# Kernel tuning notes

Hardware: AMD Instinct MI355X
Metric: run time of the kernel (lower is better)

The kernel has to match this reference:

```python
import jax, jax.numpy as jnp
import numpy as np

N, E, F, H, C, L = 50000, 800000, 32, 4, 32, 3
HC = H * C
NEG = 0.2  # leaky_relu negative slope (GATv2Conv default and explicit LeakyReLU(0.2))


def _gat_layer(x, src, dst, ea, Wl, bl, Wr, br, att, We, cb, lW, lb, bsc, bsh):
    # GATv2 linear transforms: [N, F] -> [N, H, C]
    xl = (x @ Wl + bl).reshape(N, H, C)
    xr = (x @ Wr + br).reshape(N, H, C)
    xj = xl[src]            # [E, H, C] messages from source nodes
    xi = xr[dst]            # [E, H, C] target-side features
    ep = (ea[:, None] @ We).reshape(E, H, C)  # edge-linear, edge_dim=1
    e = jax.nn.leaky_relu(xi + xj + ep, NEG)
    logits = jnp.einsum('ehc,hc->eh', e, att)            # [E, H]
    # segment softmax over destination node neighborhoods
    m = jax.ops.segment_max(logits, dst, num_segments=N)
    a = jnp.exp(logits - m[dst])
    denom = jax.ops.segment_sum(a, dst, num_segments=N)
    alpha = a / denom[dst]                               # [E, H]
    msg = xj * alpha[..., None]                          # [E, H, C]
    out = jax.ops.segment_sum(msg, dst, num_segments=N).reshape(N, HC) + cb
    # trailing per-layer MLP: Linear -> LeakyReLU(0.2) -> BatchNorm1d (eval, affine)
    h = jax.nn.leaky_relu(out @ lW + lb, NEG)
    return h * bsc + bsh


def setup_inputs() -> dict:
    key = jax.random.key(0)
    ks = jax.random.split(key, 24)
    s = 0.1
    inp = {
        'x': jax.random.normal(ks[0], (N, F), jnp.float32),
        'edge_index': jax.random.randint(ks[1], (2, E), 0, N, jnp.int32),
        'edge_attr': jax.random.normal(ks[2], (E,), jnp.float32),
        'batch': jnp.zeros((N,), jnp.int32),
        # stacked per-layer conv params (all 3 layers share shapes: F==hidden)
        'Wl': jax.random.normal(ks[3], (L, F, HC), jnp.float32) * s,
        'bl': jnp.zeros((L, HC), jnp.float32),
        'Wr': jax.random.normal(ks[4], (L, F, HC), jnp.float32) * s,
        'br': jnp.zeros((L, HC), jnp.float32),
        'att': jax.random.normal(ks[5], (L, H, C), jnp.float32) * s,
        'We': jax.random.normal(ks[6], (L, 1, HC), jnp.float32) * s,
        'conv_b': jnp.zeros((L, HC), jnp.float32),
        'lin_W': jax.random.normal(ks[7], (L, HC, F), jnp.float32) * s,
        'lin_b': jnp.zeros((L, F), jnp.float32),
        'bn_scale': jnp.ones((L, F), jnp.float32),
        'bn_shift': jnp.zeros((L, F), jnp.float32),
        # fcn head: hidden -> 256 -> 32 -> num_classes
        'W1': jax.random.normal(ks[8], (F, 256), jnp.float32) * s,
        'b1': jnp.zeros((256,), jnp.float32),
        'W2': jax.random.normal(ks[9], (256, 32), jnp.float32) * s,
        'b2': jnp.zeros((32,), jnp.float32),
        'W3': jax.random.normal(ks[10], (32, 2), jnp.float32) * s,
        'b3': jnp.zeros((2,), jnp.float32),
    }
    return inp


def reference(x, edge_index, edge_attr, batch, Wl, bl, Wr, br, att, We, conv_b,
              lin_W, lin_b, bn_scale, bn_shift, W1, b1, W2, b2, W3, b3):
    src, dst = edge_index[0], edge_index[1]
    ea = jnp.abs(edge_attr)
    h = x
    for i in range(L):
        h = _gat_layer(h, src, dst, ea, Wl[i], bl[i], Wr[i], br[i], att[i],
                       We[i], conv_b[i], lin_W[i], lin_b[i], bn_scale[i], bn_shift[i])
    # global mean pool over graphs in batch (single graph here, B=1)
    B = 1
    sums = jax.ops.segment_sum(h, batch, num_segments=B)
    cnts = jax.ops.segment_sum(jnp.ones((N, 1), h.dtype), batch, num_segments=B)
    g = sums / cnts
    g = jax.nn.leaky_relu(g @ W1 + b1, NEG)
    g = jax.nn.leaky_relu(g @ W2 + b2, NEG)
    return g @ W3 + b3
```

## Files before the change

kernel.cpp:

```cpp
#include <hip/hip_runtime.h>
#include <hip/hip_bf16.h>
#include <math.h>

#define NN 50000
#define EE 800000
#define HC 128
#define FF 32
#define NEG 0.2f
#define CAP 64
#define LOG2E 1.4426950408889634f


__global__ void k_bucket(const int* __restrict__ src, const int* __restrict__ dst,
                         const float* __restrict__ ea, int* __restrict__ cnt,
                         int2* __restrict__ pairs) {
    int e = blockIdx.x * 256 + threadIdx.x;
    if (e >= EE) return;
    int d = dst[e];
    int pos = atomicAdd(&cnt[d], 1);
    pairs[d * CAP + pos] = make_int2(src[e], __float_as_int(fabsf(ea[e])));
}


__global__ void k_hist(const int* __restrict__ dst, int* __restrict__ deg) {
    int e = blockIdx.x * 256 + threadIdx.x;
    if (e < EE) atomicAdd(&deg[dst[e]], 1);
}

__global__ void k_scan1(const int* __restrict__ deg, int* __restrict__ part) {
    __shared__ int sd[256];
    int b = blockIdx.x, t = threadIdx.x;
    int base = b * 1024 + t * 4;
    int s = 0;
#pragma unroll
    for (int i = 0; i < 4; ++i) { int idx = base + i; if (idx < NN) s += deg[idx]; }
    sd[t] = s; __syncthreads();
    for (int off = 128; off; off >>= 1) { if (t < off) sd[t] += sd[t + off]; __syncthreads(); }
    if (t == 0) part[b] = sd[0];
}

__global__ void k_scan2(int* __restrict__ part, int nb) {
    if (threadIdx.x == 0) {
        int run = 0;
        for (int i = 0; i < nb; ++i) { int v = part[i]; part[i] = run; run += v; }
    }
}

__global__ void k_scan3(const int* __restrict__ deg, const int* __restrict__ part,
                        int* __restrict__ rowptr) {
    __shared__ int sd[256];
    int b = blockIdx.x, t = threadIdx.x;
    int base = b * 1024 + t * 4;
    int v[4]; int mine = 0;
#pragma unroll
    for (int i = 0; i < 4; ++i) { int idx = base + i; v[i] = (idx < NN) ? deg[idx] : 0; mine += v[i]; }
    sd[t] = mine; __syncthreads();
    for (int off = 1; off < 256; off <<= 1) {
        int tmp = (t >= off) ? sd[t - off] : 0;
        __syncthreads();
        sd[t] += tmp;
        __syncthreads();
    }
    int run = sd[t] - mine + part[b];
#pragma unroll
    for (int i = 0; i < 4; ++i) { int idx = base + i; if (idx < NN) rowptr[idx] = run; run += v[i]; }
    if (b == 0 && t == 0) rowptr[NN] = EE;
}

__global__ void k_scatter(const int* __restrict__ src, const int* __restrict__ dst,
                          const float* __restrict__ ea, const int* __restrict__ rowptr,
                          int* __restrict__ fill, int2* __restrict__ pairs) {
    int e = blockIdx.x * 256 + threadIdx.x;
    if (e >= EE) return;
    int d = dst[e];
    int pos = rowptr[d] + atomicAdd(&fill[d], 1);
    pairs[pos] = make_int2(src[e], __float_as_int(fabsf(ea[e])));
}


__global__ __launch_bounds__(256) void k_dual_linear(
        const float* __restrict__ x,
        const float* __restrict__ Wl, const float* __restrict__ bl,
        const float* __restrict__ Wr, const float* __restrict__ br,
        float* __restrict__ xl, float* __restrict__ xr) {
    const int t = threadIdx.x;
    const int l = t & 63;
    const int half = l >> 5;
    const int lc = l & 31;
    const float* __restrict__ W  = half ? Wr : Wl;
    const float* __restrict__ bb = half ? br : bl;
    float* __restrict__ outp     = half ? xr : xl;

    float4 w[32];
#pragma unroll
    for (int k = 0; k < 32; ++k)
        w[k] = *(const float4*)(W + k * 128 + 4 * lc);
    const float4 bias = *(const float4*)(bb + 4 * lc);

    const int gw = blockIdx.x * 4 + (t >> 6);
    const int nW = gridDim.x * 4;
    const int q8 = 4 * (l & 7);

    int n = gw;
    if (n >= NN) return;
    float4 r0 = *(const float4*)(x + (size_t)n * 32 + q8);
    int n1 = n + nW < NN ? n + nW : n;
    float4 r1 = *(const float4*)(x + (size_t)n1 * 32 + q8);

    for (; n < NN; n += nW) {
        float4 cur = r0;
        r0 = r1;
        int np = n + 2 * nW < NN ? n + 2 * nW : n;
        r1 = *(const float4*)(x + (size_t)np * 32 + q8);

        float4 acc = bias;
#pragma unroll
        for (int q = 0; q < 8; ++q) {
            float vx = __shfl(cur.x, q, 8);
            float vy = __shfl(cur.y, q, 8);
            float vz = __shfl(cur.z, q, 8);
            float vw = __shfl(cur.w, q, 8);
            acc.x = fmaf(vx, w[4 * q + 0].x, acc.x);
            acc.y = fmaf(vx, w[4 * q + 0].y, acc.y);
            acc.z = fmaf(vx, w[4 * q + 0].z, acc.z);
            acc.w = fmaf(vx, w[4 * q + 0].w, acc.w);
            acc.x = fmaf(vy, w[4 * q + 1].x, acc.x);
            acc.y = fmaf(vy, w[4 * q + 1].y, acc.y);
            acc.z = fmaf(vy, w[4 * q + 1].z, acc.z);
            acc.w = fmaf(vy, w[4 * q + 1].w, acc.w);
            acc.x = fmaf(vz, w[4 * q + 2].x, acc.x);
            acc.y = fmaf(vz, w[4 * q + 2].y, acc.y);
            acc.z = fmaf(vz, w[4 * q + 2].z, acc.z);
            acc.w = fmaf(vz, w[4 * q + 2].w, acc.w);
            acc.x = fmaf(vw, w[4 * q + 3].x, acc.x);
            acc.y = fmaf(vw, w[4 * q + 3].y, acc.y);
            acc.z = fmaf(vw, w[4 * q + 3].z, acc.z);
            acc.w = fmaf(vw, w[4 * q + 3].w, acc.w);
        }
        *(float4*)(outp + (size_t)n * 128 + 4 * lc) = acc;
    }
}


template<bool BUCKET>
__global__ __launch_bounds__(256) void k_gat_agg(
        const float* __restrict__ xl, const float* __restrict__ xr,
        const int* __restrict__ idx,
        const int2* __restrict__ pairs,
        const float* __restrict__ att,
        const float* __restrict__ Wev,
        const float* __restrict__ cb,
        float* __restrict__ outb) {
    const int l = threadIdx.x & 31;
    const int n = blockIdx.x * 8 + (threadIdx.x >> 5);
    const char* __restrict__ xlp = (const char*)xl + (l << 4);

    float4 att4 = ((const float4*)att)[l];
    att4.x *= LOG2E; att4.y *= LOG2E; att4.z *= LOG2E; att4.w *= LOG2E;
    float4 we4  = ((const float4*)Wev)[l];
    float4 xr4  = ((const float4*)xr)[n * 32 + l];
    int beg, end;
    if (BUCKET) { beg = n * CAP; end = beg + idx[n]; }
    else        { beg = idx[n];  end = idx[n + 1]; }
    const int last = end - 1;

    float m = -INFINITY, s = 0.f;
    float4 acc = make_float4(0.f, 0.f, 0.f, 0.f);

    if (beg < end) {
        int2 p0 = pairs[beg];
        int2 p1 = pairs[beg + 1 < last ? beg + 1 : last];
        int2 p2 = pairs[beg + 2 < last ? beg + 2 : last];
        float4 x0 = *(const float4*)(xlp + (p0.x << 9));
        float4 x1 = *(const float4*)(xlp + (p1.x << 9));

#pragma unroll 2
        for (int j = beg; j <= last; ++j) {
            int jn = j + 3 < last ? j + 3 : last;
            int2 pn = pairs[jn];
            float4 xn = *(const float4*)(xlp + (p2.x << 9));

            float sea = __int_as_float(p0.y);
            float4 v;
            v.x = fmaf(sea, we4.x, xr4.x + x0.x);
            v.y = fmaf(sea, we4.y, xr4.y + x0.y);
            v.z = fmaf(sea, we4.z, xr4.z + x0.z);
            v.w = fmaf(sea, we4.w, xr4.w + x0.w);
            v.x = fmaxf(v.x, NEG * v.x);
            v.y = fmaxf(v.y, NEG * v.y);
            v.z = fmaxf(v.z, NEG * v.z);
            v.w = fmaxf(v.w, NEG * v.w);
            float pl = v.x * att4.x;
            pl = fmaf(v.y, att4.y, pl);
            pl = fmaf(v.z, att4.z, pl);
            pl = fmaf(v.w, att4.w, pl);
            pl += __shfl_xor(pl, 4);
            pl += __shfl_xor(pl, 2);
            pl += __shfl_xor(pl, 1);

            float mn = fmaxf(m, pl);
            float c  = __builtin_amdgcn_exp2f(m - mn);
            float e  = __builtin_amdgcn_exp2f(pl - mn);
            s = fmaf(s, c, e);
            acc.x = fmaf(acc.x, c, e * x0.x);
            acc.y = fmaf(acc.y, c, e * x0.y);
            acc.z = fmaf(acc.z, c, e * x0.z);
            acc.w = fmaf(acc.w, c, e * x0.w);
            m = mn;

            p0 = p1; p1 = p2; p2 = pn;
            x0 = x1; x1 = xn;
        }
    }

    float inv = (s > 0.f) ? 1.f / s : 0.f;
    float4 cb4 = ((const float4*)cb)[l];
    float4 o;
    o.x = fmaf(acc.x, inv, cb4.x);
    o.y = fmaf(acc.y, inv, cb4.y);
    o.z = fmaf(acc.z, inv, cb4.z);
    o.w = fmaf(acc.w, inv, cb4.w);
    ((float4*)outb)[n * 32 + l] = o;
}


__global__ __launch_bounds__(256) void k_mlp_bn(
        const float* __restrict__ outb,
        const float* __restrict__ lW, const float* __restrict__ lb,
        const float* __restrict__ bsc, const float* __restrict__ bsh,
        float* __restrict__ h) {
    const int t = threadIdx.x;
    const int l = t & 63;
    const int half = l >> 5;
    const int cg = (l >> 2) & 7;
    const int kg = l & 3;

    float4 w[32];
#pragma unroll
    for (int kl = 0; kl < 32; ++kl)
        w[kl] = *(const float4*)(lW + (size_t)(32 * kg + kl) * 32 + 4 * cg);

    const float4 bias = (kg == 0) ? *(const float4*)(lb + 4 * cg)
                                  : make_float4(0.f, 0.f, 0.f, 0.f);
    const float4 sc4 = *(const float4*)(bsc + 4 * cg);
    const float4 sh4 = *(const float4*)(bsh + 4 * cg);

    const int gw = blockIdx.x * 4 + (t >> 6);
    const int nW = gridDim.x * 4;
    const int quad = 4 * (l & 31);
    const int kg8 = kg * 8;

    int p = gw;
    if (p >= NN / 2) return;
    float4 r0 = *(const float4*)(outb + (size_t)(2 * p + half) * 128 + quad);
    int p1i = p + nW < NN / 2 ? p + nW : p;
    float4 r1 = *(const float4*)(outb + (size_t)(2 * p1i + half) * 128 + quad);

    for (; p < NN / 2; p += nW) {
        float4 cur = r0;
        r0 = r1;
        int pp = p + 2 * nW < NN / 2 ? p + 2 * nW : p;
        r1 = *(const float4*)(outb + (size_t)(2 * pp + half) * 128 + quad);

        float4 acc = bias;
#pragma unroll
        for (int j = 0; j < 8; ++j) {
            float vx = __shfl(cur.x, kg8 + j, 32);
            float vy = __shfl(cur.y, kg8 + j, 32);
            float vz = __shfl(cur.z, kg8 + j, 32);
            float vw = __shfl(cur.w, kg8 + j, 32);
            acc.x = fmaf(vx, w[4 * j + 0].x, acc.x);
            acc.y = fmaf(vx, w[4 * j + 0].y, acc.y);
            acc.z = fmaf(vx, w[4 * j + 0].z, acc.z);
            acc.w = fmaf(vx, w[4 * j + 0].w, acc.w);
            acc.x = fmaf(vy, w[4 * j + 1].x, acc.x);
            acc.y = fmaf(vy, w[4 * j + 1].y, acc.y);
            acc.z = fmaf(vy, w[4 * j + 1].z, acc.z);
            acc.w = fmaf(vy, w[4 * j + 1].w, acc.w);
            acc.x = fmaf(vz, w[4 * j + 2].x, acc.x);
            acc.y = fmaf(vz, w[4 * j + 2].y, acc.y);
            acc.z = fmaf(vz, w[4 * j + 2].z, acc.z);
            acc.w = fmaf(vz, w[4 * j + 2].w, acc.w);
            acc.x = fmaf(vw, w[4 * j + 3].x, acc.x);
            acc.y = fmaf(vw, w[4 * j + 3].y, acc.y);
            acc.z = fmaf(vw, w[4 * j + 3].z, acc.z);
            acc.w = fmaf(vw, w[4 * j + 3].w, acc.w);
        }
        acc.x += __shfl_xor(acc.x, 1); acc.x += __shfl_xor(acc.x, 2);
        acc.y += __shfl_xor(acc.y, 1); acc.y += __shfl_xor(acc.y, 2);
        acc.z += __shfl_xor(acc.z, 1); acc.z += __shfl_xor(acc.z, 2);
        acc.w += __shfl_xor(acc.w, 1); acc.w += __shfl_xor(acc.w, 2);

        if (kg == 0) {
            float4 o;
            o.x = fmaxf(acc.x, NEG * acc.x);
            o.y = fmaxf(acc.y, NEG * acc.y);
            o.z = fmaxf(acc.z, NEG * acc.z);
            o.w = fmaxf(acc.w, NEG * acc.w);
            o.x = fmaf(o.x, sc4.x, sh4.x);
            o.y = fmaf(o.y, sc4.y, sh4.y);
            o.z = fmaf(o.z, sc4.z, sh4.z);
            o.w = fmaf(o.w, sc4.w, sh4.w);
            *(float4*)(h + (size_t)(2 * p + half) * 32 + 4 * cg) = o;
        }
    }
}


__global__ void k_colsum(const float* __restrict__ h, float* __restrict__ part_g) {
    __shared__ float sd[256];
    int t = threadIdx.x;
    int col = t & 31, r = t >> 5;
    float local = 0.f;
    for (int row = blockIdx.x * 8 + r; row < NN; row += gridDim.x * 8)
        local += h[row * FF + col];
    sd[t] = local; __syncthreads();
    if (r < 4) sd[t] += sd[t + 128];
    __syncthreads();
    if (r < 2) sd[t] += sd[t + 64];
    __syncthreads();
    if (r < 1) part_g[blockIdx.x * 32 + col] = sd[t] + sd[t + 32];
}


__global__ void k_head(const float* __restrict__ part_g,
                       const float* __restrict__ W1, const float* __restrict__ b1,
                       const float* __restrict__ W2, const float* __restrict__ b2,
                       const float* __restrict__ W3, const float* __restrict__ b3,
                       float* __restrict__ out) {
    __shared__ float red[256];
    __shared__ float gv[32];
    __shared__ float h1[256];
    __shared__ float h2[32];
    int t = threadIdx.x;
    int col = t & 31, r = t >> 5;
    float lsum = 0.f;
#pragma unroll
    for (int k = 0; k < 16; ++k) lsum += part_g[(r + 8 * k) * 32 + col];
    red[t] = lsum; __syncthreads();
    if (r < 4) red[t] += red[t + 128];
    __syncthreads();
    if (r < 2) red[t] += red[t + 64];
    __syncthreads();
    if (r < 1) gv[col] = (red[t] + red[t + 32]) * (1.0f / NN);
    __syncthreads();
    float acc = b1[t];
#pragma unroll 8
    for (int k = 0; k < 32; ++k) acc += gv[k] * W1[k * 256 + t];
    h1[t] = acc > 0.f ? acc : NEG * acc;
    __syncthreads();
    if (t < 32) {
        float a = b2[t];
        for (int k = 0; k < 256; ++k) a += h1[k] * W2[k * 32 + t];
        h2[t] = a > 0.f ? a : NEG * a;
    }
    __syncthreads();
    if (t < 2) {
        float a = b3[t];
#pragma unroll
        for (int k = 0; k < 32; ++k) a += h2[k] * W3[k * 2 + t];
        out[t] = a;
    }
}


static inline size_t alignup(size_t x) { return (x + 255) & ~size_t(255); }

extern "C" void kernel_launch(void* const* d_in, const int* in_sizes, int n_in,
                              void* d_out, int out_size, void* d_ws, size_t ws_size,
                              hipStream_t stream) {
    const float* x     = (const float*)d_in[0];
    const int*   eidx  = (const int*)d_in[1];
    const float* eattr = (const float*)d_in[2];
    const float* Wl    = (const float*)d_in[4];
    const float* bl    = (const float*)d_in[5];
    const float* Wr    = (const float*)d_in[6];
    const float* br    = (const float*)d_in[7];
    const float* att   = (const float*)d_in[8];
    const float* We    = (const float*)d_in[9];
    const float* cb    = (const float*)d_in[10];
    const float* lW    = (const float*)d_in[11];
    const float* lb    = (const float*)d_in[12];
    const float* bsc   = (const float*)d_in[13];
    const float* bsh   = (const float*)d_in[14];
    const float* W1    = (const float*)d_in[15];
    const float* b1    = (const float*)d_in[16];
    const float* W2    = (const float*)d_in[17];
    const float* b2    = (const float*)d_in[18];
    const float* W3    = (const float*)d_in[19];
    const float* b3    = (const float*)d_in[20];

    const int* srcp = eidx;
    const int* dstp = eidx + EE;

    char* ws = (char*)d_ws;
    size_t off = 0;
    float* xl     = (float*)(ws + off); off += alignup((size_t)NN * HC * 4);
    float* xr     = (float*)(ws + off); off += alignup((size_t)NN * HC * 4);
    float* outb   = (float*)(ws + off); off += alignup((size_t)NN * HC * 4);
    float* hA     = (float*)(ws + off); off += alignup((size_t)NN * FF * 4);
    float* hB     = (float*)(ws + off); off += alignup((size_t)NN * FF * 4);
    float* part_g = (float*)(ws + off); off += alignup(128 * 32 * 4);

    size_t boff = off;
    int2*  pairsB = (int2*)(ws + boff); boff += alignup((size_t)NN * CAP * 8);
    int*   cntB   = (int*) (ws + boff); boff += alignup((size_t)NN * 4);
    const bool bucket = (ws_size >= boff);

    const float* cur = x;
    float* hbuf[2] = {hA, hB};

    if (bucket) {
        hipMemsetAsync(cntB, 0, (size_t)NN * 4, stream);
        k_bucket<<<(EE + 255) / 256, 256, 0, stream>>>(srcp, dstp, eattr, cntB, pairsB);
        for (int i = 0; i < 3; ++i) {
            k_dual_linear<<<768, 256, 0, stream>>>(cur, Wl + i * FF * HC, bl + i * HC,
                                                   Wr + i * FF * HC, br + i * HC, xl, xr);
            k_gat_agg<true><<<NN / 8, 256, 0, stream>>>(xl, xr, cntB, pairsB,
                                                        att + i * HC, We + i * HC,
                                                        cb + i * HC, outb);
            k_mlp_bn<<<768, 256, 0, stream>>>(outb, lW + i * HC * FF, lb + i * FF,
                                              bsc + i * FF, bsh + i * FF, hbuf[i & 1]);
            cur = hbuf[i & 1];
        }
    } else {
        size_t coff = off;
        int2* pairsC  = (int2*)(ws + coff); coff += alignup((size_t)EE * 8);
        int*  rowptr  = (int*) (ws + coff); coff += alignup((size_t)(NN + 1) * 4);
        int*  deg     = (int*) (ws + coff); coff += alignup((size_t)NN * 4);
        int*  fill    = (int*) (ws + coff); coff += alignup((size_t)NN * 4);
        int*  part    = (int*) (ws + coff); coff += alignup(64 * 4);

        hipMemsetAsync(deg, 0, alignup((size_t)NN * 4) + (size_t)NN * 4, stream);
        const int nChunk = (NN + 1023) / 1024;
        k_hist<<<(EE + 255) / 256, 256, 0, stream>>>(dstp, deg);
        k_scan1<<<nChunk, 256, 0, stream>>>(deg, part);
        k_scan2<<<1, 64, 0, stream>>>(part, nChunk);
        k_scan3<<<nChunk, 256, 0, stream>>>(deg, part, rowptr);
        k_scatter<<<(EE + 255) / 256, 256, 0, stream>>>(srcp, dstp, eattr, rowptr, fill, pairsC);

        for (int i = 0; i < 3; ++i) {
            k_dual_linear<<<768, 256, 0, stream>>>(cur, Wl + i * FF * HC, bl + i * HC,
                                                   Wr + i * FF * HC, br + i * HC, xl, xr);
            k_gat_agg<false><<<NN / 8, 256, 0, stream>>>(xl, xr, rowptr, pairsC,
                                                         att + i * HC, We + i * HC,
                                                         cb + i * HC, outb);
            k_mlp_bn<<<768, 256, 0, stream>>>(outb, lW + i * HC * FF, lb + i * FF,
                                              bsc + i * FF, bsh + i * FF, hbuf[i & 1]);
            cur = hbuf[i & 1];
        }
    }

    k_colsum<<<128, 256, 0, stream>>>(cur, part_g);
    k_head<<<1, 256, 0, stream>>>(part_g, W1, b1, W2, b2, W3, b3, (float*)d_out);
}
```

Before: 513.8 us.

## Fuse GAT aggregation with per-layer MLP/BN and final mean-pool colsum

The per-layer MLP+LeakyReLU+BatchNorm is folded into the GAT aggregation kernel, with the 128x32 weight staged in shared memory, so the [N,128] intermediate buffer is never written or read back. On the last layer the node outputs are reduced into shared-memory column sums and atomically added into 64 partial rows, which removes the separate colsum kernel and the final h write. The online softmax now uses a single exp2 per edge by selecting between rescale and new weight. The cost is extra shared-memory weight loads per block, less occupancy, and float atomics that make the pooled sum order nondeterministic.

```diff
diff --git a/kernel.cpp b/kernel.cpp
--- a/kernel.cpp
+++ b/kernel.cpp
@@ -142,15 +142,29 @@
 }
 
 
-template<bool BUCKET>
-__global__ __launch_bounds__(256) void k_gat_agg(
+template<bool BUCKET, bool LAST>
+__global__ __launch_bounds__(256) void k_gat_mlp(
         const float* __restrict__ xl, const float* __restrict__ xr,
         const int* __restrict__ idx,
         const int2* __restrict__ pairs,
         const float* __restrict__ att,
         const float* __restrict__ Wev,
         const float* __restrict__ cb,
-        float* __restrict__ outb) {
+        const float* __restrict__ lW,
+        const float* __restrict__ lb,
+        const float* __restrict__ bsc, const float* __restrict__ bsh,
+        float* __restrict__ hout,
+        float* __restrict__ part_g) {
+    __shared__ float sW[HC * FF];
+    __shared__ float gp[FF];
+    {
+        float4* d4 = (float4*)sW;
+        const float4* s4 = (const float4*)lW;
+        for (int i = threadIdx.x; i < HC * FF / 4; i += 256) d4[i] = s4[i];
+        if (LAST && threadIdx.x < 32) gp[threadIdx.x] = 0.f;
+    }
+    __syncthreads();
+
     const int l = threadIdx.x & 31;
     const int n = blockIdx.x * 8 + (threadIdx.x >> 5);
     const char* __restrict__ xlp = (const char*)xl + (l << 4);
@@ -199,8 +213,10 @@
             pl += __shfl_xor(pl, 1);
 
             float mn = fmaxf(m, pl);
-            float c  = __builtin_amdgcn_exp2f(m - mn);
-            float e  = __builtin_amdgcn_exp2f(pl - mn);
+            float d  = __builtin_amdgcn_exp2f(fminf(m, pl) - mn);
+            bool up  = pl > m;
+            float c  = up ? d : 1.0f;
+            float e  = up ? 1.0f : d;
             s = fmaf(s, c, e);
             acc.x = fmaf(acc.x, c, e * x0.x);
             acc.y = fmaf(acc.y, c, e * x0.y);
@@ -220,106 +236,63 @@
     o.y = fmaf(acc.y, inv, cb4.y);
     o.z = fmaf(acc.z, inv, cb4.z);
     o.w = fmaf(acc.w, inv, cb4.w);
-    ((float4*)outb)[n * 32 + l] = o;
-}
-
-
-__global__ __launch_bounds__(256) void k_mlp_bn(
-        const float* __restrict__ outb,
-        const float* __restrict__ lW, const float* __restrict__ lb,
-        const float* __restrict__ bsc, const float* __restrict__ bsh,
-        float* __restrict__ h) {
-    const int t = threadIdx.x;
-    const int l = t & 63;
-    const int half = l >> 5;
+
     const int cg = (l >> 2) & 7;
     const int kg = l & 3;
-
-    float4 w[32];
-#pragma unroll
-    for (int kl = 0; kl < 32; ++kl)
-        w[kl] = *(const float4*)(lW + (size_t)(32 * kg + kl) * 32 + 4 * cg);
-
-    const float4 bias = (kg == 0) ? *(const float4*)(lb + 4 * cg)
-                                  : make_float4(0.f, 0.f, 0.f, 0.f);
-    const float4 sc4 = *(const float4*)(bsc + 4 * cg);
-    const float4 sh4 = *(const float4*)(bsh + 4 * cg);
-
-    const int gw = blockIdx.x * 4 + (t >> 6);
-    const int nW = gridDim.x * 4;
-    const int quad = 4 * (l & 31);
     const int kg8 = kg * 8;
-
-    int p = gw;
-    if (p >= NN / 2) return;
-    float4 r0 = *(const float4*)(outb + (size_t)(2 * p + half) * 128 + quad);
-    int p1i = p + nW < NN / 2 ? p + nW : p;
-    float4 r1 = *(const float4*)(outb + (size_t)(2 * p1i + half) * 128 + quad);
-
-    for (; p < NN / 2; p += nW) {
-        float4 cur = r0;
-        r0 = r1;
-        int pp = p + 2 * nW < NN / 2 ? p + 2 * nW : p;
-        r1 = *(const float4*)(outb + (size_t)(2 * pp + half) * 128 + quad);
-
-        float4 acc = bias;
-#pragma unroll
-        for (int j = 0; j < 8; ++j) {
-            float vx = __shfl(cur.x, kg8 + j, 32);
-            float vy = __shfl(cur.y, kg8 + j, 32);
-            float vz = __shfl(cur.z, kg8 + j, 32);
-            float vw = __shfl(cur.w, kg8 + j, 32);
-            acc.x = fmaf(vx, w[4 * j + 0].x, acc.x);
-            acc.y = fmaf(vx, w[4 * j + 0].y, acc.y);
-            acc.z = fmaf(vx, w[4 * j + 0].z, acc.z);
-            acc.w = fmaf(vx, w[4 * j + 0].w, acc.w);
-            acc.x = fmaf(vy, w[4 * j + 1].x, acc.x);
-            acc.y = fmaf(vy, w[4 * j + 1].y, acc.y);
-            acc.z = fmaf(vy, w[4 * j + 1].z, acc.z);
-            acc.w = fmaf(vy, w[4 * j + 1].w, acc.w);
-            acc.x = fmaf(vz, w[4 * j + 2].x, acc.x);
-            acc.y = fmaf(vz, w[4 * j + 2].y, acc.y);
-            acc.z = fmaf(vz, w[4 * j + 2].z, acc.z);
-            acc.w = fmaf(vz, w[4 * j + 2].w, acc.w);
-            acc.x = fmaf(vw, w[4 * j + 3].x, acc.x);
-            acc.y = fmaf(vw, w[4 * j + 3].y, acc.y);
-            acc.z = fmaf(vw, w[4 * j + 3].z, acc.z);
-            acc.w = fmaf(vw, w[4 * j + 3].w, acc.w);
+    float4 a2 = (kg == 0) ? *(const float4*)(lb + 4 * cg)
+                          : make_float4(0.f, 0.f, 0.f, 0.f);
+#pragma unroll
+    for (int j = 0; j < 8; ++j) {
+        float vx = __shfl(o.x, kg8 + j, 32);
+        float vy = __shfl(o.y, kg8 + j, 32);
+        float vz = __shfl(o.z, kg8 + j, 32);
+        float vw = __shfl(o.w, kg8 + j, 32);
+        const float* wp = sW + (32 * kg + 4 * j) * 32 + 4 * cg;
+        float4 w0 = *(const float4*)(wp);
+        float4 w1 = *(const float4*)(wp + 32);
+        float4 w2 = *(const float4*)(wp + 64);
+        float4 w3 = *(const float4*)(wp + 96);
+        a2.x = fmaf(vx, w0.x, a2.x); a2.y = fmaf(vx, w0.y, a2.y);
+        a2.z = fmaf(vx, w0.z, a2.z); a2.w = fmaf(vx, w0.w, a2.w);
+        a2.x = fmaf(vy, w1.x, a2.x); a2.y = fmaf(vy, w1.y, a2.y);
+        a2.z = fmaf(vy, w1.z, a2.z); a2.w = fmaf(vy, w1.w, a2.w);
+        a2.x = fmaf(vz, w2.x, a2.x); a2.y = fmaf(vz, w2.y, a2.y);
+        a2.z = fmaf(vz, w2.z, a2.z); a2.w = fmaf(vz, w2.w, a2.w);
+        a2.x = fmaf(vw, w3.x, a2.x); a2.y = fmaf(vw, w3.y, a2.y);
+        a2.z = fmaf(vw, w3.z, a2.z); a2.w = fmaf(vw, w3.w, a2.w);
+    }
+    a2.x += __shfl_xor(a2.x, 1); a2.x += __shfl_xor(a2.x, 2);
+    a2.y += __shfl_xor(a2.y, 1); a2.y += __shfl_xor(a2.y, 2);
+    a2.z += __shfl_xor(a2.z, 1); a2.z += __shfl_xor(a2.z, 2);
+    a2.w += __shfl_xor(a2.w, 1); a2.w += __shfl_xor(a2.w, 2);
+
+    if (kg == 0) {
+        const float4 sc4 = *(const float4*)(bsc + 4 * cg);
+        const float4 sh4 = *(const float4*)(bsh + 4 * cg);
+        float4 hq;
+        hq.x = fmaxf(a2.x, NEG * a2.x);
+        hq.y = fmaxf(a2.y, NEG * a2.y);
+        hq.z = fmaxf(a2.z, NEG * a2.z);
+        hq.w = fmaxf(a2.w, NEG * a2.w);
+        hq.x = fmaf(hq.x, sc4.x, sh4.x);
+        hq.y = fmaf(hq.y, sc4.y, sh4.y);
+        hq.z = fmaf(hq.z, sc4.z, sh4.z);
+        hq.w = fmaf(hq.w, sc4.w, sh4.w);
+        if (LAST) {
+            atomicAdd(&gp[4 * cg + 0], hq.x);
+            atomicAdd(&gp[4 * cg + 1], hq.y);
+            atomicAdd(&gp[4 * cg + 2], hq.z);
+            atomicAdd(&gp[4 * cg + 3], hq.w);
+        } else {
+            *(float4*)(hout + (size_t)n * 32 + 4 * cg) = hq;
         }
-        acc.x += __shfl_xor(acc.x, 1); acc.x += __shfl_xor(acc.x, 2);
-        acc.y += __shfl_xor(acc.y, 1); acc.y += __shfl_xor(acc.y, 2);
-        acc.z += __shfl_xor(acc.z, 1); acc.z += __shfl_xor(acc.z, 2);
-        acc.w += __shfl_xor(acc.w, 1); acc.w += __shfl_xor(acc.w, 2);
-
-        if (kg == 0) {
-            float4 o;
-            o.x = fmaxf(acc.x, NEG * acc.x);
-            o.y = fmaxf(acc.y, NEG * acc.y);
-            o.z = fmaxf(acc.z, NEG * acc.z);
-            o.w = fmaxf(acc.w, NEG * acc.w);
-            o.x = fmaf(o.x, sc4.x, sh4.x);
-            o.y = fmaf(o.y, sc4.y, sh4.y);
-            o.z = fmaf(o.z, sc4.z, sh4.z);
-            o.w = fmaf(o.w, sc4.w, sh4.w);
-            *(float4*)(h + (size_t)(2 * p + half) * 32 + 4 * cg) = o;
-        }
-    }
-}
-
-
-__global__ void k_colsum(const float* __restrict__ h, float* __restrict__ part_g) {
-    __shared__ float sd[256];
-    int t = threadIdx.x;
-    int col = t & 31, r = t >> 5;
-    float local = 0.f;
-    for (int row = blockIdx.x * 8 + r; row < NN; row += gridDim.x * 8)
-        local += h[row * FF + col];
-    sd[t] = local; __syncthreads();
-    if (r < 4) sd[t] += sd[t + 128];
-    __syncthreads();
-    if (r < 2) sd[t] += sd[t + 64];
-    __syncthreads();
-    if (r < 1) part_g[blockIdx.x * 32 + col] = sd[t] + sd[t + 32];
+    }
+    if (LAST) {
+        __syncthreads();
+        if (threadIdx.x < 32)
+            atomicAdd(&part_g[(blockIdx.x & 63) * 32 + threadIdx.x], gp[threadIdx.x]);
+    }
 }
 
 
@@ -336,7 +309,7 @@
     int col = t & 31, r = t >> 5;
     float lsum = 0.f;
 #pragma unroll
-    for (int k = 0; k < 16; ++k) lsum += part_g[(r + 8 * k) * 32 + col];
+    for (int k = 0; k < 8; ++k) lsum += part_g[(r + 8 * k) * 32 + col];
     red[t] = lsum; __syncthreads();
     if (r < 4) red[t] += red[t + 128];
     __syncthreads();
@@ -395,43 +368,51 @@
 
     char* ws = (char*)d_ws;
     size_t off = 0;
-    float* xl     = (float*)(ws + off); off += alignup((size_t)NN * HC * 4);
-    float* xr     = (float*)(ws + off); off += alignup((size_t)NN * HC * 4);
-    float* outb   = (float*)(ws + off); off += alignup((size_t)NN * HC * 4);
-    float* hA     = (float*)(ws + off); off += alignup((size_t)NN * FF * 4);
-    float* hB     = (float*)(ws + off); off += alignup((size_t)NN * FF * 4);
-    float* part_g = (float*)(ws + off); off += alignup(128 * 32 * 4);
+    float* xl = (float*)(ws + off); off += alignup((size_t)NN * HC * 4);
+    float* xr = (float*)(ws + off); off += alignup((size_t)NN * HC * 4);
+    float* hA = (float*)(ws + off); off += alignup((size_t)NN * FF * 4);
+    float* hB = (float*)(ws + off); off += alignup((size_t)NN * FF * 4);
 
     size_t boff = off;
-    int2*  pairsB = (int2*)(ws + boff); boff += alignup((size_t)NN * CAP * 8);
-    int*   cntB   = (int*) (ws + boff); boff += alignup((size_t)NN * 4);
+    int2*  pairsB = (int2*) (ws + boff); boff += alignup((size_t)NN * CAP * 8);
+    int*   cntB   = (int*)  (ws + boff); size_t z0 = boff; boff += alignup((size_t)NN * 4);
+    float* partGB = (float*)(ws + boff); boff += alignup(64 * 32 * 4);
+    const size_t zlenB = boff - z0;
     const bool bucket = (ws_size >= boff);
 
     const float* cur = x;
     float* hbuf[2] = {hA, hB};
 
     if (bucket) {
-        hipMemsetAsync(cntB, 0, (size_t)NN * 4, stream);
+        hipMemsetAsync(cntB, 0, zlenB, stream);
         k_bucket<<<(EE + 255) / 256, 256, 0, stream>>>(srcp, dstp, eattr, cntB, pairsB);
         for (int i = 0; i < 3; ++i) {
             k_dual_linear<<<768, 256, 0, stream>>>(cur, Wl + i * FF * HC, bl + i * HC,
                                                    Wr + i * FF * HC, br + i * HC, xl, xr);
-            k_gat_agg<true><<<NN / 8, 256, 0, stream>>>(xl, xr, cntB, pairsB,
-                                                        att + i * HC, We + i * HC,
-                                                        cb + i * HC, outb);
-            k_mlp_bn<<<768, 256, 0, stream>>>(outb, lW + i * HC * FF, lb + i * FF,
-                                              bsc + i * FF, bsh + i * FF, hbuf[i & 1]);
+            if (i < 2)
+                k_gat_mlp<true, false><<<NN / 8, 256, 0, stream>>>(
+                    xl, xr, cntB, pairsB, att + i * HC, We + i * HC, cb + i * HC,
+                    lW + i * HC * FF, lb + i * FF, bsc + i * FF, bsh + i * FF,
+                    hbuf[i & 1], partGB);
+            else
+                k_gat_mlp<true, true><<<NN / 8, 256, 0, stream>>>(
+                    xl, xr, cntB, pairsB, att + i * HC, We + i * HC, cb + i * HC,
+                    lW + i * HC * FF, lb + i * FF, bsc + i * FF, bsh + i * FF,
+                    hbuf[i & 1], partGB);
             cur = hbuf[i & 1];
         }
+        k_head<<<1, 256, 0, stream>>>(partGB, W1, b1, W2, b2, W3, b3, (float*)d_out);
     } else {
         size_t coff = off;
-        int2* pairsC  = (int2*)(ws + coff); coff += alignup((size_t)EE * 8);
-        int*  rowptr  = (int*) (ws + coff); coff += alignup((size_t)(NN + 1) * 4);
-        int*  deg     = (int*) (ws + coff); coff += alignup((size_t)NN * 4);
-        int*  fill    = (int*) (ws + coff); coff += alignup((size_t)NN * 4);
-        int*  part    = (int*) (ws + coff); coff += alignup(64 * 4);
-
-        hipMemsetAsync(deg, 0, alignup((size_t)NN * 4) + (size_t)NN * 4, stream);
+        int2*  pairsC = (int2*) (ws + coff); coff += alignup((size_t)EE * 8);
+        int*   rowptr = (int*)  (ws + coff); coff += alignup((size_t)(NN + 1) * 4);
+        int*   deg    = (int*)  (ws + coff); size_t z1 = coff; coff += alignup((size_t)NN * 4);
+        int*   fill   = (int*)  (ws + coff); coff += alignup((size_t)NN * 4);
+        int*   part   = (int*)  (ws + coff); coff += alignup(64 * 4);
+        float* partGC = (float*)(ws + coff); coff += alignup(64 * 32 * 4);
+        const size_t zlenC = coff - z1;
+
+        hipMemsetAsync(deg, 0, zlenC, stream);
         const int nChunk = (NN + 1023) / 1024;
         k_hist<<<(EE + 255) / 256, 256, 0, stream>>>(dstp, deg);
         k_scan1<<<nChunk, 256, 0, stream>>>(deg, part);
@@ -442,15 +423,18 @@
         for (int i = 0; i < 3; ++i) {
             k_dual_linear<<<768, 256, 0, stream>>>(cur, Wl + i * FF * HC, bl + i * HC,
                                                    Wr + i * FF * HC, br + i * HC, xl, xr);
-            k_gat_agg<false><<<NN / 8, 256, 0, stream>>>(xl, xr, rowptr, pairsC,
-                                                         att + i * HC, We + i * HC,
-                                                         cb + i * HC, outb);
-            k_mlp_bn<<<768, 256, 0, stream>>>(outb, lW + i * HC * FF, lb + i * FF,
-                                              bsc + i * FF, bsh + i * FF, hbuf[i & 1]);
+            if (i < 2)
+                k_gat_mlp<false, false><<<NN / 8, 256, 0, stream>>>(
+                    xl, xr, rowptr, pairsC, att + i * HC, We + i * HC, cb + i * HC,
+                    lW + i * HC * FF, lb + i * FF, bsc + i * FF, bsh + i * FF,
+                    hbuf[i & 1], partGC);
+            else
+                k_gat_mlp<false, true><<<NN / 8, 256, 0, stream>>>(
+                    xl, xr, rowptr, pairsC, att + i * HC, We + i * HC, cb + i * HC,
+                    lW + i * HC * FF, lb + i * FF, bsc + i * FF, bsh + i * FF,
+                    hbuf[i & 1], partGC);
             cur = hbuf[i & 1];
         }
-    }
-
-    k_colsum<<<128, 256, 0, stream>>>(cur, part_g);
-    k_head<<<1, 256, 0, stream>>>(part_g, W1, b1, W2, b2, W3, b3, (float*)d_out);
-}
+        k_head<<<1, 256, 0, stream>>>(partGC, W1, b1, W2, b2, W3, b3, (float*)d_out);
+    }
+}
```

Measured after the change: 465.6 us. 1.1x faster.
